# Kernel optimization log

Hardware: AMD Instinct MI355X
Metric: run time of the kernel (lower is better)

The kernel has to match this reference:

```python
import jax, jax.numpy as jnp
import numpy as np

# module hyperparams (init_kwargs)
IN_SIZE = 64      # D
OUT_SIZE = 64     # D_
NUM_CLUSTER = 8   # K
HEADS = 4         # H
GAMMA = 1.0
TAU = 10.0

E = 400000        # num edges
N_NODES = 50000


def setup_inputs() -> dict:
    key = jax.random.key(0)
    ks = jax.random.split(key, 8)
    msg = jax.random.normal(ks[0], (E, OUT_SIZE), dtype=jnp.float32)
    x_i = jax.random.normal(ks[1], (E, IN_SIZE), dtype=jnp.float32)
    x_j = jax.random.normal(ks[2], (E, IN_SIZE), dtype=jnp.float32)
    e_ij = jax.random.normal(ks[3], (E, IN_SIZE), dtype=jnp.float32)
    index = jax.random.randint(ks[4], (E,), 0, N_NODES, dtype=jnp.int32)
    # xavier-uniform-ish cluster centers [H, K, D]
    lim = float(np.sqrt(6.0 / (NUM_CLUSTER + IN_SIZE)))
    k = jax.random.uniform(ks[5], (HEADS, NUM_CLUSTER, IN_SIZE), dtype=jnp.float32,
                           minval=-lim, maxval=lim)
    # final Linear(K*D_ -> D_), stored as [in, out]
    limw = float(np.sqrt(1.0 / (NUM_CLUSTER * OUT_SIZE)))
    W = jax.random.uniform(ks[6], (NUM_CLUSTER * OUT_SIZE, OUT_SIZE), dtype=jnp.float32,
                           minval=-limw, maxval=limw)
    b = jax.random.uniform(ks[7], (OUT_SIZE,), dtype=jnp.float32, minval=-limw, maxval=limw)
    return {"msg": msg, "x_i": x_i, "x_j": x_j, "e_ij": e_ij, "index": index,
            "num_nodes": N_NODES, "k": k, "W": W, "b": b}


def reference(msg, x_i, x_j, e_ij, index, num_nodes, k, W, b):
    H, K, D, D_ = HEADS, NUM_CLUSTER, IN_SIZE, OUT_SIZE
    # agg_q = elementwise sum of neighbor features and edge features -> [E, D]
    x = x_j + e_ij
    kf = k.reshape(H * K, D)
    # squared euclidean distances: [H*K, E]
    dist = (jnp.sum(kf * kf, axis=1)[:, None]
            + jnp.sum(x * x, axis=1)[None, :]
            - 2.0 * (kf @ x.T))
    dist = jnp.maximum(dist, 0.0)
    # Student-t kernel
    t = (1.0 + dist / GAMMA) ** (-(GAMMA + 1.0) / 2.0)
    t = t.reshape(H, K, -1).transpose(2, 1, 0)  # [E, K, H]
    w = t / jnp.sum(t, axis=1, keepdims=True) * TAU  # normalize over clusters
    w = jax.nn.softmax(jnp.mean(w, axis=-1), axis=-1)  # [E, K]
    # weight messages per cluster -> [E, K*D_]
    new_msg = (w[:, :, None] * msg[:, None, :]).reshape(-1, K * D_)
    agg = jax.ops.segment_sum(new_msg, index, num_segments=num_nodes)  # [N, K*D_]
    out = agg @ W + b
    return jax.nn.leaky_relu(out, negative_slope=0.01)
```

## Files before the change

kernel.cpp:

```cpp
#include <hip/hip_runtime.h>
#include <hip/hip_bf16.h>

typedef unsigned short u16;
typedef unsigned int   u32;

typedef __attribute__((ext_vector_type(8))) short  short8;
typedef __attribute__((ext_vector_type(4))) float  floatx4;

__device__ __forceinline__ u32 rne_pack(float lo, float hi) {
  u32 bl = __float_as_uint(lo), bh = __float_as_uint(hi);
  u32 rl = ((bl + 0x7FFFu + ((bl >> 16) & 1u)) >> 16) & 0xFFFFu;
  u32 rh = (bh + 0x7FFFu + ((bh >> 16) & 1u)) & 0xFFFF0000u;
  return rl | rh;
}

__device__ __forceinline__ short8 scale_frag(uint4 mraw, float w) {
  const u32* in = (const u32*)&mraw;
  uint4 o; u32* ou = (u32*)&o;
  #pragma unroll
  for (int i = 0; i < 4; ++i) {
    float lo = __uint_as_float(in[i] << 16) * w;
    float hi = __uint_as_float(in[i]) * w;
    ou[i] = __builtin_amdgcn_perm(__float_as_uint(hi), __float_as_uint(lo), 0x07060302u);
  }
  return *(short8*)&o;
}

__global__ __launch_bounds__(256, 2) void fused_kernel(
    const float* __restrict__ msg, const float* __restrict__ xj,
    const float* __restrict__ eij, const float* __restrict__ kc,
    const float* __restrict__ Wg, const int* __restrict__ idx,
    float* __restrict__ out, int E) {
  __shared__ __align__(16) char un[65536];
  float* tl = (float*)un;
  u16*   Wl = (u16*)un;
  __shared__ __align__(16) float wsm[2048];
  __shared__ float kn[32];

  const int tid  = threadIdx.x;
  const int lane = tid & 63, wv = tid >> 6;
  const int ln   = lane & 15, q  = lane >> 4;
  const int e0   = blockIdx.x * 256;

  const float4* kc4 = (const float4*)kc;
  short8 af[2][2];
  float knp[2] = {0.f, 0.f};
  #pragma unroll
  for (int mt = 0; mt < 2; ++mt) {
    #pragma unroll
    for (int kk = 0; kk < 2; ++kk) {
      size_t b4 = (size_t)(mt * 16 + ln) * 16 + kk * 8 + q * 2;
      float4 c0 = kc4[b4], c1 = kc4[b4 + 1];
      knp[mt] += c0.x*c0.x + c0.y*c0.y + c0.z*c0.z + c0.w*c0.w
               + c1.x*c1.x + c1.y*c1.y + c1.z*c1.z + c1.w*c1.w;
      u32 pk[4] = { rne_pack(c0.x, c0.y), rne_pack(c0.z, c0.w),
                    rne_pack(c1.x, c1.y), rne_pack(c1.z, c1.w) };
      af[mt][kk] = *(short8*)pk;
    }
    float s = knp[mt];
    s += __shfl_xor(s, 16);
    s += __shfl_xor(s, 32);
    if (wv == 0 && q == 0) kn[mt * 16 + ln] = s;
  }

  const float4* xj4  = (const float4*)xj;
  const float4* eij4 = (const float4*)eij;
  #pragma unroll
  for (int g = 0; g < 4; ++g) {
    int el = wv * 64 + g * 16 + ln;
    int ge = e0 + el; if (ge >= E) ge = 0;
    size_t b4 = (size_t)ge * 16 + q * 2;
    float4 x0 = xj4[b4],     x1 = xj4[b4 + 1];
    float4 x2 = xj4[b4 + 8], x3 = xj4[b4 + 9];
    float4 ea0 = eij4[b4],     ea1 = eij4[b4 + 1];
    float4 ea2 = eij4[b4 + 8], ea3 = eij4[b4 + 9];
    float s0x = x0.x+ea0.x, s0y = x0.y+ea0.y, s0z = x0.z+ea0.z, s0w = x0.w+ea0.w;
    float s1x = x1.x+ea1.x, s1y = x1.y+ea1.y, s1z = x1.z+ea1.z, s1w = x1.w+ea1.w;
    float s2x = x2.x+ea2.x, s2y = x2.y+ea2.y, s2z = x2.z+ea2.z, s2w = x2.w+ea2.w;
    float s3x = x3.x+ea3.x, s3y = x3.y+ea3.y, s3z = x3.z+ea3.z, s3w = x3.w+ea3.w;
    float ps = s0x*s0x + s0y*s0y + s0z*s0z + s0w*s0w
             + s1x*s1x + s1y*s1y + s1z*s1z + s1w*s1w
             + s2x*s2x + s2y*s2y + s2z*s2z + s2w*s2w
             + s3x*s3x + s3y*s3y + s3z*s3z + s3w*s3w;
    u32 p0[4] = { rne_pack(s0x, s0y), rne_pack(s0z, s0w),
                  rne_pack(s1x, s1y), rne_pack(s1z, s1w) };
    u32 p1[4] = { rne_pack(s2x, s2y), rne_pack(s2z, s2w),
                  rne_pack(s3x, s3y), rne_pack(s3z, s3w) };
    ps += __shfl_xor(ps, 16);
    ps += __shfl_xor(ps, 32);
    short8 bb0 = *(short8*)p0, bb1 = *(short8*)p1;
    floatx4 acc0 = {0.f,0.f,0.f,0.f}, acc1 = {0.f,0.f,0.f,0.f};
    acc0 = __builtin_amdgcn_mfma_f32_16x16x32_bf16(af[0][0], bb0, acc0, 0, 0, 0);
    acc0 = __builtin_amdgcn_mfma_f32_16x16x32_bf16(af[0][1], bb1, acc0, 0, 0, 0);
    acc1 = __builtin_amdgcn_mfma_f32_16x16x32_bf16(af[1][0], bb0, acc1, 0, 0, 0);
    acc1 = __builtin_amdgcn_mfma_f32_16x16x32_bf16(af[1][1], bb1, acc1, 0, 0, 0);
    #pragma unroll
    for (int i = 0; i < 4; ++i) {
      tl[el * 33 + (q * 4 + i)]      = acc0[i];
      tl[el * 33 + 16 + (q * 4 + i)] = acc1[i];
    }
    if (q == 0) tl[el * 33 + 32] = ps;
  }
  __syncthreads();

  {
    int e = tid;
    bool valid = (e0 + e) < E;
    float xn = tl[e * 33 + 32];
    float tv[32];
    float hs[4] = {0.f, 0.f, 0.f, 0.f};
    #pragma unroll
    for (int c = 0; c < 32; ++c) {
      float dist = kn[c] + xn - 2.f * tl[e * 33 + c];
      dist = dist > 0.f ? dist : 0.f;
      float t = 1.f / (1.f + dist);
      tv[c] = t;
      hs[c >> 3] += t;
    }
    float r0 = 1.f / hs[0], r1 = 1.f / hs[1], r2 = 1.f / hs[2], r3 = 1.f / hs[3];
    float m[8], mx = -1e30f;
    #pragma unroll
    for (int k = 0; k < 8; ++k) {
      m[k] = 2.5f * (tv[k] * r0 + tv[8 + k] * r1 + tv[16 + k] * r2 + tv[24 + k] * r3);
      mx = m[k] > mx ? m[k] : mx;
    }
    float p[8], sum = 0.f;
    #pragma unroll
    for (int k = 0; k < 8; ++k) { p[k] = __expf(m[k] - mx); sum += p[k]; }
    float rs = valid ? (1.f / sum) : 0.f;
    floatx4 w0 = {p[0]*rs, p[1]*rs, p[2]*rs, p[3]*rs};
    floatx4 w1 = {p[4]*rs, p[5]*rs, p[6]*rs, p[7]*rs};
    *(floatx4*)&wsm[e * 8]     = w0;
    *(floatx4*)&wsm[e * 8 + 4] = w1;
  }
  __syncthreads();

  #pragma unroll
  for (int it = 0; it < 16; ++it) {
    int c  = (tid >> 6) + it * 4;
    int kk = c >> 2, q2 = c & 3, n = tid & 63;
    const float* src = Wg + (size_t)(kk * 32 + q2 * 8) * 64 + n;
    u32 pk[4];
    #pragma unroll
    for (int jp = 0; jp < 4; ++jp)
      pk[jp] = rne_pack(src[(jp * 2) * 64], src[(jp * 2 + 1) * 64]);
    *(uint4*)&Wl[(c * 64 + n) * 8] = *(uint4*)pk;
  }

  const float4* msg4 = (const float4*)msg;
  uint4 mf[4][2];
  const int edgebase = e0 + wv * 64;
  #pragma unroll
  for (int s = 0; s < 4; ++s) {
    int eg = edgebase + s * 16 + ln; if (eg >= E) eg = E - 1;
    size_t mb = (size_t)eg * 16 + q * 2;
    #pragma unroll
    for (int h = 0; h < 2; ++h) {
      float4 m0 = msg4[mb + h * 8], m1 = msg4[mb + h * 8 + 1];
      u32 pk[4] = { rne_pack(m0.x, m0.y), rne_pack(m0.z, m0.w),
                    rne_pack(m1.x, m1.y), rne_pack(m1.z, m1.w) };
      mf[s][h] = *(uint4*)pk;
    }
  }
  floatx4 wf[4][2];
  #pragma unroll
  for (int s = 0; s < 4; ++s) {
    int eL = wv * 64 + s * 16 + ln;
    wf[s][0] = *(floatx4*)&wsm[eL * 8];
    wf[s][1] = *(floatx4*)&wsm[eL * 8 + 4];
  }
  floatx4 acc[4][4];
  #pragma unroll
  for (int s = 0; s < 4; ++s)
    #pragma unroll
    for (int t = 0; t < 4; ++t) { floatx4 z = {0.f,0.f,0.f,0.f}; acc[s][t] = z; }
  __syncthreads();

  #pragma unroll
  for (int kb = 0; kb < 8; ++kb) {
    float wsc[4];
    #pragma unroll
    for (int s = 0; s < 4; ++s) wsc[s] = wf[s][kb >> 2][kb & 3];
    #pragma unroll
    for (int hh = 0; hh < 2; ++hh) {
      int kk = kb * 2 + hh;
      short8 bfr[4];
      #pragma unroll
      for (int t = 0; t < 4; ++t)
        bfr[t] = *(short8*)&Wl[((kk * 4 + q) * 64 + t * 16 + ln) * 8];
      #pragma unroll
      for (int s = 0; s < 4; ++s) {
        short8 a = scale_frag(mf[s][hh], wsc[s]);
        #pragma unroll
        for (int t = 0; t < 4; ++t)
          acc[s][t] = __builtin_amdgcn_mfma_f32_16x16x32_bf16(a, bfr[t], acc[s][t], 0, 0, 0);
      }
    }
  }

  #pragma unroll
  for (int s = 0; s < 4; ++s) {
    #pragma unroll
    for (int i = 0; i < 4; ++i) {
      int eg = edgebase + s * 16 + q * 4 + i;
      if (eg < E) {
        int node = idx[eg];
        float* dst = &out[(size_t)node * 64 + ln];
        #pragma unroll
        for (int t = 0; t < 4; ++t) unsafeAtomicAdd(dst + t * 16, acc[s][t][i]);
      }
    }
  }
}

__global__ __launch_bounds__(256) void finish_kernel(
    float* __restrict__ out, const float* __restrict__ b, int n4) {
  int i = blockIdx.x * 256 + threadIdx.x;
  if (i >= n4) return;
  float4 v = ((const float4*)out)[i];
  int cb = (i & 15) * 4;
  v.x += b[cb];     v.x = v.x > 0.f ? v.x : 0.01f * v.x;
  v.y += b[cb + 1]; v.y = v.y > 0.f ? v.y : 0.01f * v.y;
  v.z += b[cb + 2]; v.z = v.z > 0.f ? v.z : 0.01f * v.z;
  v.w += b[cb + 3]; v.w = v.w > 0.f ? v.w : 0.01f * v.w;
  ((float4*)out)[i] = v;
}

extern "C" void kernel_launch(void* const* d_in, const int* in_sizes, int n_in,
                              void* d_out, int out_size, void* d_ws, size_t ws_size,
                              hipStream_t stream) {
  const float* msg = (const float*)d_in[0];
  const float* xj  = (const float*)d_in[2];
  const float* eij = (const float*)d_in[3];
  const int*   idx = (const int*)d_in[4];
  const float* kc  = (const float*)d_in[6];
  const float* Wg  = (const float*)d_in[7];
  const float* bg  = (const float*)d_in[8];

  int E    = in_sizes[0] / 64;
  int Nout = out_size;
  float* out = (float*)d_out;

  hipMemsetAsync(out, 0, (size_t)Nout * 4, stream);

  int blocks = (E + 255) / 256;
  fused_kernel<<<blocks, 256, 0, stream>>>(msg, xj, eij, kc, Wg, idx, out, E);

  int n4 = Nout / 4;
  finish_kernel<<<(n4 + 255) / 256, 256, 0, stream>>>(out, bg, n4);
}
```

Baseline: 417.4 us.

## Scatter outputs as packed fixed-point 64-bit integer atomics

Replaces the four float atomic adds per edge row with two 64-bit integer atomics. Each carries two 32-bit fixed-point values offset by a bias, and the W columns in shared memory are permuted so each lane holds an adjacent column pair. A new finish kernel works out the per-node edge count from the accumulated bias, subtracts it, converts back to float, and applies the bias and leaky ReLU. This halves the atomic count, at the cost of fixed-point quantization, a risk of overflow or carry between the packed halves, and dependence on the bias-based count recovery.

```diff
diff --git a/kernel.cpp b/kernel.cpp
--- a/kernel.cpp
+++ b/kernel.cpp
@@ -3,9 +3,14 @@
 
 typedef unsigned short u16;
 typedef unsigned int   u32;
+typedef unsigned long long u64;
 
 typedef __attribute__((ext_vector_type(8))) short  short8;
 typedef __attribute__((ext_vector_type(4))) float  floatx4;
+
+#define FIX_SCALE 65536.0f
+#define FIX_INV   (1.0f / 65536.0f)
+#define FIX_BIAS  (1 << 26)
 
 __device__ __forceinline__ u32 rne_pack(float lo, float hi) {
   u32 bl = __float_as_uint(lo), bh = __float_as_uint(hi);
@@ -30,7 +35,7 @@
     const float* __restrict__ msg, const float* __restrict__ xj,
     const float* __restrict__ eij, const float* __restrict__ kc,
     const float* __restrict__ Wg, const int* __restrict__ idx,
-    float* __restrict__ out, int E) {
+    u64* __restrict__ o64, int E) {
   __shared__ __align__(16) char un[65536];
   float* tl = (float*)un;
   u16*   Wl = (u16*)un;
@@ -144,7 +149,9 @@
     #pragma unroll
     for (int jp = 0; jp < 4; ++jp)
       pk[jp] = rne_pack(src[(jp * 2) * 64], src[(jp * 2 + 1) * 64]);
-    *(uint4*)&Wl[(c * 64 + n) * 8] = *(uint4*)pk;
+    int tt = (n & 1) + ((n >> 5) << 1);
+    int mm = tt * 16 + ((n & 31) >> 1);
+    *(uint4*)&Wl[(c * 64 + mm) * 8] = *(uint4*)pk;
   }
 
   const float4* msg4 = (const float4*)msg;
@@ -205,25 +212,39 @@
       int eg = edgebase + s * 16 + q * 4 + i;
       if (eg < E) {
         int node = idx[eg];
-        float* dst = &out[(size_t)node * 64 + ln];
-        #pragma unroll
-        for (int t = 0; t < 4; ++t) unsafeAtomicAdd(dst + t * 16, acc[s][t][i]);
+        u64* dst = o64 + (size_t)node * 32 + ln;
+        u32 l0 = (u32)((int)rintf(acc[s][0][i] * FIX_SCALE) + FIX_BIAS);
+        u32 h0 = (u32)((int)rintf(acc[s][1][i] * FIX_SCALE) + FIX_BIAS);
+        u32 l1 = (u32)((int)rintf(acc[s][2][i] * FIX_SCALE) + FIX_BIAS);
+        u32 h1 = (u32)((int)rintf(acc[s][3][i] * FIX_SCALE) + FIX_BIAS);
+        atomicAdd(dst,      ((u64)h0 << 32) | l0);
+        atomicAdd(dst + 16, ((u64)h1 << 32) | l1);
       }
     }
   }
 }
 
-__global__ __launch_bounds__(256) void finish_kernel(
-    float* __restrict__ out, const float* __restrict__ b, int n4) {
-  int i = blockIdx.x * 256 + threadIdx.x;
-  if (i >= n4) return;
-  float4 v = ((const float4*)out)[i];
-  int cb = (i & 15) * 4;
-  v.x += b[cb];     v.x = v.x > 0.f ? v.x : 0.01f * v.x;
-  v.y += b[cb + 1]; v.y = v.y > 0.f ? v.y : 0.01f * v.y;
-  v.z += b[cb + 2]; v.z = v.z > 0.f ? v.z : 0.01f * v.z;
-  v.w += b[cb + 3]; v.w = v.w > 0.f ? v.w : 0.01f * v.w;
-  ((float4*)out)[i] = v;
+__global__ __launch_bounds__(256) void finish_packed(
+    u64* __restrict__ a64, const float* __restrict__ b, int ng) {
+  int g = blockIdx.x * 256 + threadIdx.x;
+  if (g >= ng) return;
+  int node = g >> 3, pg = g & 7;
+  u64* ap = a64 + (size_t)node * 32 + pg * 4;
+  ulonglong4 v = *(ulonglong4*)ap;
+  u32 w[8] = { (u32)v.x, (u32)(v.x >> 32), (u32)v.y, (u32)(v.y >> 32),
+               (u32)v.z, (u32)(v.z >> 32), (u32)v.w, (u32)(v.w >> 32) };
+  u32 cnt = (w[0] + (1u << 25)) >> 26;
+  u32 cb  = cnt << 26;
+  int col0 = pg * 8;
+  float r[8];
+  #pragma unroll
+  for (int c = 0; c < 8; ++c) {
+    float z = (float)(int)(w[c] - cb) * FIX_INV + b[col0 + c];
+    r[c] = z > 0.f ? z : 0.01f * z;
+  }
+  float* op = (float*)a64 + (size_t)node * 64 + col0;
+  *(float4*)op       = make_float4(r[0], r[1], r[2], r[3]);
+  *(float4*)(op + 4) = make_float4(r[4], r[5], r[6], r[7]);
 }
 
 extern "C" void kernel_launch(void* const* d_in, const int* in_sizes, int n_in,
@@ -244,8 +265,9 @@
   hipMemsetAsync(out, 0, (size_t)Nout * 4, stream);
 
   int blocks = (E + 255) / 256;
-  fused_kernel<<<blocks, 256, 0, stream>>>(msg, xj, eij, kc, Wg, idx, out, E);
-
-  int n4 = Nout / 4;
-  finish_kernel<<<(n4 + 255) / 256, 256, 0, stream>>>(out, bg, n4);
-}
+  fused_kernel<<<blocks, 256, 0, stream>>>(msg, xj, eij, kc, Wg, idx,
+                                           (u64*)out, E);
+
+  int ng = Nout / 8;
+  finish_packed<<<(ng + 255) / 256, 256, 0, stream>>>((u64*)out, bg, ng);
+}
```

New measurement: 408.1 us. -2.2%, faster.
